# Optimization experiments

Hardware: AMD Instinct MI355X
Metric: run time of the kernel (lower is better)

Reference implementation:

```python
import jax, jax.numpy as jnp
import numpy as np

THRESH = 8000.0  # saturating partial-sum accumulator threshold (thresh=8000 in source)
GROUP = 128      # channel chunk size used by split_tensor_* helpers
EPS = 1e-5

def binarize(x):
    # sign() forward with straight-through estimator (standard BinarizeConv2d behavior)
    return x + jax.lax.stop_gradient(jnp.sign(x) - x)

def psum_conv3x3(x, w):
    """3x3 'same' conv computed as 9 shifted-window partial sums per 128-channel
    group, with the running accumulator saturated to [-THRESH, THRESH] after each
    partial sum (emulating a low-bit hardware accumulator).
    x: [B, C, H, W]; w: [O, C, 3, 3] -> out [B, O, H, W]."""
    B, C, H, W = x.shape
    O = w.shape[0]
    xp = jnp.pad(x, ((0, 0), (0, 0), (1, 1), (1, 1)))
    acc = jnp.zeros((B, O, H, W), dtype=x.dtype)
    n_groups = C // GROUP
    for g in range(n_groups):
        xg = xp[:, g * GROUP:(g + 1) * GROUP]
        wg = w[:, g * GROUP:(g + 1) * GROUP]
        # split_tensor ordering: x1..x9 vary row (dim2) fastest, then col (dim3)
        for col in range(3):
            for row in range(3):
                part = jnp.einsum('bchw,oc->bohw',
                                  xg[:, :, row:row + H, col:col + W],
                                  wg[:, :, row, col])
                acc = jnp.clip(acc + part, -THRESH, THRESH)
    return acc

def batchnorm(x, gamma, beta, mean, var):
    inv = gamma / jnp.sqrt(var + EPS)
    return x * inv[None, :, None, None] + (beta - mean * inv)[None, :, None, None]

def setup_inputs() -> dict:
    key = jax.random.key(0)
    ks = jax.random.split(key, 12)
    B, C, H, W = 64, 128, 56, 56
    return {
        'x': jax.random.normal(ks[0], (B, C, H, W), jnp.float32),
        'w1': jax.random.normal(ks[1], (C, C, 3, 3), jnp.float32),
        'w2': jax.random.normal(ks[2], (C, C, 3, 3), jnp.float32),
        'gamma1': jax.random.uniform(ks[3], (C,), jnp.float32, 0.5, 1.5),
        'beta1': jax.random.normal(ks[4], (C,), jnp.float32) * 0.1,
        'mean1': jax.random.normal(ks[5], (C,), jnp.float32),
        'var1': jax.random.uniform(ks[6], (C,), jnp.float32, 0.5, 1.5),
        'gamma2': jax.random.uniform(ks[7], (C,), jnp.float32, 0.5, 1.5),
        'beta2': jax.random.normal(ks[8], (C,), jnp.float32) * 0.1,
        'mean2': jax.random.normal(ks[9], (C,), jnp.float32),
        'var2': jax.random.uniform(ks[10], (C,), jnp.float32, 0.5, 1.5),
    }

def reference(x, w1, w2, gamma1, beta1, mean1, var1, gamma2, beta2, mean2, var2):
    residual = x
    out = psum_conv3x3(binarize(x), binarize(w1))
    out = batchnorm(out, gamma1, beta1, mean1, var1)
    out = jnp.clip(out, -1.0, 1.0)  # hardtanh
    out = psum_conv3x3(binarize(out), binarize(w2))
    out = batchnorm(out, gamma2, beta2, mean2, var2)
    out = out + residual
    out = jnp.clip(out, -1.0, 1.0)
    return out
```

## Files before the change

### kernel.cpp

```cpp
#include <hip/hip_runtime.h>
#include <cstdint>
#include <cstddef>


typedef int      v4i __attribute__((ext_vector_type(4)));
typedef float    v4f __attribute__((ext_vector_type(4)));
typedef unsigned int v2u __attribute__((ext_vector_type(2)));

constexpr int B = 64, C = 128, H = 56, W = 56;
constexpr int HP = H + 2, WP = W + 2;
constexpr int PIX = H * W;
constexpr int M = B * H * W;
constexpr int NTILES = M / 256;
constexpr int TPX = NTILES / 8;

constexpr size_t XS_BYTES = (size_t)B * HP * WP * C;
constexpr size_t XS1_OFF = 0;
constexpr size_t XS2_OFF = XS_BYTES;
constexpr size_t WF_BYTES = 18 * 8192;
constexpr size_t WF1_OFF = 2 * XS_BYTES;
constexpr size_t WF2_OFF = WF1_OFF + WF_BYTES;
constexpr size_t BNP_OFF = WF2_OFF + WF_BYTES;

__global__ __launch_bounds__(256) void zero_halo(int8_t* __restrict__ xs1,
                                                 int8_t* __restrict__ xs2) {
    int b = blockIdx.x >> 2;
    int q = blockIdx.x & 3;
    int t = q * 256 + threadIdx.x;
    size_t ib = (size_t)b * HP * WP * C;
#pragma unroll
    for (int a = 0; a < 2; ++a) {
        uint32_t* p = (uint32_t*)((a ? xs2 : xs1) + ib);
        const int ROWD = WP * C / 4;
        for (int i = t; i < ROWD; i += 1024) {
            p[i] = 0;
            p[(HP - 1) * ROWD + i] = 0;
        }
        for (int i = t; i < 56 * 2 * 32; i += 1024) {
            int r = i >> 6;
            int side = (i >> 5) & 1;
            int j = i & 31;
            p[((r + 1) * WP + side * (WP - 1)) * (C / 4) + j] = 0;
        }
    }
}

__global__ __launch_bounds__(256) void prep_x(const float* __restrict__ x,
                                              int8_t* __restrict__ xs) {
    __shared__ uint32_t tl[256 * 33];
    int t = threadIdx.x;
    int m = blockIdx.x * 256 + t;
    int b_ = m / PIX, hw = m % PIX;
    const float* xp = x + (size_t)b_ * C * PIX + hw;
#pragma unroll
    for (int c4 = 0; c4 < 32; ++c4) {
        uint32_t v = 0;
#pragma unroll
        for (int j = 0; j < 4; ++j) {
            float f = __builtin_nontemporal_load(xp + (size_t)(c4 * 4 + j) * PIX);
            v |= ((uint32_t)(uint8_t)(int8_t)((f > 0.f) - (f < 0.f))) << (8 * j);
        }
        tl[t * 33 + c4] = v;
    }
    __syncthreads();
    int pl = t >> 3, co = t & 7;
#pragma unroll
    for (int pass = 0; pass < 8; ++pass) {
        int p = pass * 32 + pl;
        int mg = blockIdx.x * 256 + p;
        int b2 = mg / PIX, hw2 = mg % PIX, h2 = hw2 / W, w2 = hw2 % W;
        size_t ob = ((size_t)(b2 * HP + h2 + 1) * WP + (w2 + 1)) * C + co * 16;
        v4i val;
#pragma unroll
        for (int k = 0; k < 4; ++k) val[k] = (int)tl[p * 33 + co * 4 + k];
        *(v4i*)(xs + ob) = val;
    }
}

__global__ __launch_bounds__(256) void prep_w(
    const float* __restrict__ w1, const float* __restrict__ w2,
    const float* __restrict__ g1, const float* __restrict__ be1,
    const float* __restrict__ mu1, const float* __restrict__ va1,
    const float* __restrict__ g2, const float* __restrict__ be2,
    const float* __restrict__ mu2, const float* __restrict__ va2,
    int8_t* __restrict__ wf1, int8_t* __restrict__ wf2,
    float* __restrict__ bnp) {
    int t = blockIdx.x * 256 + threadIdx.x;
    if (t < 256) {
        int o = t & 127;
        if (t < 128) {
            float inv = g1[o] / sqrtf(va1[o] + 1e-5f);
            bnp[o]       = inv;
            bnp[128 + o] = __fsub_rn(be1[o], __fmul_rn(mu1[o], inv));
        } else {
            float inv = g2[o] / sqrtf(va2[o] + 1e-5f);
            bnp[256 + o] = inv;
            bnp[384 + o] = __fsub_rn(be2[o], __fmul_rn(mu2[o], inv));
        }
    }
    if (t >= 2 * 18 * 8 * 64) return;
    int lane = t & 63;
    int nsub = (t >> 6) & 7;
    int kh   = (t >> 9) & 1;
    int tap  = (t >> 10) % 9;
    int which = (t >> 10) / 9;
    const float* w = which ? w2 : w1;
    int8_t* wf = which ? wf2 : wf1;
    int o = (lane & 15) * 8 + nsub;
    int cbase = kh * 64 + (lane >> 4) * 16;
    int r = tap / 3, s = tap % 3;
    int slot = r * 6 + kh * 3 + s;
    int8_t frag[16];
#pragma unroll
    for (int j = 0; j < 16; ++j) {
        float f = w[((size_t)(o * C + cbase + j) * 3 + r) * 3 + s];
        frag[j] = (int8_t)((f > 0.f) - (f < 0.f));
    }
    *(v4i*)(wf + (size_t)((slot * 8 + nsub) * 64 + lane) * 16) =
        *(const v4i*)frag;
}

template <int RG>
__device__ __forceinline__ void do_conv(
    int mwave, const int8_t* __restrict__ xs, const int8_t* wlds,
    int lane, int quad, int l15, v4i (&acc)[RG][8])
{
    int abase[RG];
#pragma unroll
    for (int rg = 0; rg < RG; ++rg) {
        int ma = mwave + rg * 16 + l15;
        int wa = ma % W; int ta = ma / W; int ha = ta % H; int ba = ta / H;
        abase[rg] = ((ba * HP + ha) * WP + wa) * C + quad * 16;
    }
    int lidx = lane << 4;

#pragma unroll
    for (int rg = 0; rg < RG; ++rg)
#pragma unroll
        for (int n = 0; n < 8; ++n) acc[rg][n] = (v4i)0;

    v4i a0[RG], a1[RG], bf0[8], bf1[8];
#pragma unroll
    for (int rg = 0; rg < RG; ++rg) a0[rg] = *(const v4i*)(xs + abase[rg]);
#pragma unroll
    for (int n = 0; n < 8; ++n)
        bf0[n] = *(const v4i*)(wlds + n * 1024 + lidx);
    __builtin_amdgcn_sched_barrier(0);

    const int8_t* wl = wlds;
    int aoffr = 0;
#pragma unroll 1
    for (int r3 = 0; r3 < 3; ++r3) {
#pragma unroll
        for (int kk = 0; kk < 6; ++kk) {
            const bool last = (r3 == 2) && (kk == 5);
            if (!last) {
                const int nkh = (kk + 1 < 6) ? ((kk + 1) / 3) : 0;
                const int ns  = (kk + 1 < 6) ? ((kk + 1) % 3) : 0;
                const int rbump = (kk + 1 < 6) ? 0 : WP * C;
                int naoff = aoffr + rbump + nkh * 64 + ns * C;
                const int8_t* lb = wl + (kk + 1) * 8192;
                if (((kk + 1) & 1) == 0) {
#pragma unroll
                    for (int rg = 0; rg < RG; ++rg)
                        a0[rg] = *(const v4i*)(xs + abase[rg] + naoff);
#pragma unroll
                    for (int n = 0; n < 8; ++n)
                        bf0[n] = *(const v4i*)(lb + n * 1024 + lidx);
                } else {
#pragma unroll
                    for (int rg = 0; rg < RG; ++rg)
                        a1[rg] = *(const v4i*)(xs + abase[rg] + naoff);
#pragma unroll
                    for (int n = 0; n < 8; ++n)
                        bf1[n] = *(const v4i*)(lb + n * 1024 + lidx);
                }
            }
            __builtin_amdgcn_sched_barrier(0);
            __builtin_amdgcn_s_setprio(1);
            if ((kk & 1) == 0) {
#pragma unroll
                for (int n = 0; n < 8; ++n)
#pragma unroll
                    for (int rg = 0; rg < RG; ++rg)
                        acc[rg][n] = __builtin_amdgcn_mfma_i32_16x16x64_i8(
                            a0[rg], bf0[n], acc[rg][n], 0, 0, 0);
            } else {
#pragma unroll
                for (int n = 0; n < 8; ++n)
#pragma unroll
                    for (int rg = 0; rg < RG; ++rg)
                        acc[rg][n] = __builtin_amdgcn_mfma_i32_16x16x64_i8(
                            a1[rg], bf1[n], acc[rg][n], 0, 0, 0);
            }
            __builtin_amdgcn_s_setprio(0);
            __builtin_amdgcn_sched_barrier(0);
        }
        aoffr += WP * C;
        wl += 6 * 8192;
    }
}

template <int RG>
__device__ __forceinline__ void epi_p1(
    v4i (&acc)[RG][8], int mwave, int quad, int l15,
    const float* binv, const float* btt, int8_t* __restrict__ xs_next)
{
#pragma unroll
    for (int rg = 0; rg < RG; ++rg) {
        int m0 = mwave + rg * 16 + quad * 4;
        int w0 = m0 % W; int t0 = m0 / W; int h0 = t0 % H; int b0 = t0 / H;
        int base = ((b0 * HP + h0 + 1) * WP + (w0 + 1)) * C + l15 * 8;
#pragma unroll
        for (int i = 0; i < 4; ++i) {
            uint32_t lo = 0, hi = 0;
#pragma unroll
            for (int n = 0; n < 8; ++n) {
                float y = __fadd_rn(__fmul_rn((float)acc[rg][n][i], binv[n]), btt[n]);
                uint32_t sb = (uint8_t)(int8_t)((y > 0.f) - (y < 0.f));
                if (n < 4) lo |= sb << (8 * n);
                else       hi |= sb << (8 * (n - 4));
            }
            v2u pk; pk[0] = lo; pk[1] = hi;
            *(v2u*)(xs_next + base + i * C) = pk;
        }
    }
}

template <int RG>
__device__ __forceinline__ void epi_p2(
    v4i (&acc)[RG][8], int m0, int wv, int quad, int l15,
    const float* binv, const float* btt,
    const float* __restrict__ xres, float* __restrict__ out, float* sm)
{
    constexpr int PXB = 128 * RG;
    int t = wv * 64 + quad * 16 + l15;
#pragma unroll 1
    for (int p = 0; p < 16; ++p) {
        if (l15 == p) {
#pragma unroll
            for (int rg = 0; rg < RG; ++rg)
#pragma unroll
                for (int n = 0; n < 8; ++n) {
                    v4f v;
#pragma unroll
                    for (int i = 0; i < 4; ++i)
                        v[i] = __fadd_rn(__fmul_rn((float)acc[rg][n][i],
                                                   binv[n]), btt[n]);
                    *(v4f*)(sm + n * PXB + wv * (RG * 16) + rg * 16 + quad * 4) = v;
                }
        }
        __syncthreads();
        if (t < PXB * 2) {
            int o_local = t / (PXB / 4);
            int px4 = (t % (PXB / 4)) * 4;
            v4f s = *(const v4f*)(sm + o_local * PXB + px4);
            int m = m0 + px4;
            int b0 = m / PIX, pp = m - b0 * PIX;
            size_t gidx = ((size_t)(b0 * C + p * 8 + o_local)) * PIX + pp;
            v4f r = *(const v4f*)(xres + gidx);
            v4f z;
#pragma unroll
            for (int i = 0; i < 4; ++i)
                z[i] = fminf(fmaxf(__fadd_rn(s[i], r[i]), -1.f), 1.f);
            __builtin_nontemporal_store(z, (v4f*)(out + gidx));
        }
        __syncthreads();
    }
}

__global__ __launch_bounds__(512, 1) void conv_p1(
    const int8_t* __restrict__ xs,
    const int8_t* __restrict__ wf,
    const float* __restrict__ bnp,
    int8_t* __restrict__ xs_next)
{
    __shared__ int8_t wlds[18 * 8192];
    int t = threadIdx.x, lane = t & 63, wv = t >> 6;
    int quad = lane >> 4, l15 = lane & 15;

    {
        const v4i* g = (const v4i*)wf;
        v4i* l = (v4i*)wlds;
        for (int i = t; i < 18 * 512; i += 512) l[i] = g[i];
    }
    float binv[8], btt[8];
    {
        int o0 = l15 * 8, o1 = 128 + l15 * 8;
#pragma unroll
        for (int n = 0; n < 8; ++n) { binv[n] = bnp[o0 + n]; btt[n] = bnp[o1 + n]; }
    }
    __syncthreads();

    int xcd = blockIdx.x & 7, local = blockIdx.x >> 3;
#pragma unroll 1
    for (int tloc = local; tloc < 96; tloc += 32) {
        int mw = (xcd * TPX + tloc) * 256 + wv * 32;
        v4i acc[2][8];
        do_conv<2>(mw, xs, wlds, lane, quad, l15, acc);
        epi_p1<2>(acc, mw, quad, l15, binv, btt, xs_next);
    }
    if (local < 4) {
        int tile = xcd * TPX + 96 + (local >> 1);
        int mw = tile * 256 + (local & 1) * 128 + wv * 16;
        v4i acc[1][8];
        do_conv<1>(mw, xs, wlds, lane, quad, l15, acc);
        epi_p1<1>(acc, mw, quad, l15, binv, btt, xs_next);
    }
}

__global__ __launch_bounds__(512, 1) void conv_p2(
    const int8_t* __restrict__ xs,
    const int8_t* __restrict__ wf,
    const float* __restrict__ bnp,
    const float* __restrict__ xres,
    float* __restrict__ out)
{
    __shared__ int8_t wlds[18 * 8192];
    __shared__ float  sm[8 * 256];
    int t = threadIdx.x, lane = t & 63, wv = t >> 6;
    int quad = lane >> 4, l15 = lane & 15;

    {
        const v4i* g = (const v4i*)wf;
        v4i* l = (v4i*)wlds;
        for (int i = t; i < 18 * 512; i += 512) l[i] = g[i];
    }
    float binv[8], btt[8];
    {
        int o0 = 256 + l15 * 8, o1 = 384 + l15 * 8;
#pragma unroll
        for (int n = 0; n < 8; ++n) { binv[n] = bnp[o0 + n]; btt[n] = bnp[o1 + n]; }
    }
    __syncthreads();

    int xcd = blockIdx.x & 7, local = blockIdx.x >> 3;
#pragma unroll 1
    for (int tloc = local; tloc < 96; tloc += 32) {
        int m0 = (xcd * TPX + tloc) * 256;
        int mw = m0 + wv * 32;
        v4i acc[2][8];
        do_conv<2>(mw, xs, wlds, lane, quad, l15, acc);
        epi_p2<2>(acc, m0, wv, quad, l15, binv, btt, xres, out, sm);
    }
    if (local < 4) {
        int tile = xcd * TPX + 96 + (local >> 1);
        int m0 = tile * 256 + (local & 1) * 128;
        int mw = m0 + wv * 16;
        v4i acc[1][8];
        do_conv<1>(mw, xs, wlds, lane, quad, l15, acc);
        epi_p2<1>(acc, m0, wv, quad, l15, binv, btt, xres, out, sm);
    }
}

extern "C" void kernel_launch(void* const* d_in, const int* in_sizes, int n_in,
                              void* d_out, int out_size, void* d_ws, size_t ws_size,
                              hipStream_t stream) {
    const float* x   = (const float*)d_in[0];
    const float* w1  = (const float*)d_in[1];
    const float* w2  = (const float*)d_in[2];
    const float* g1  = (const float*)d_in[3];
    const float* be1 = (const float*)d_in[4];
    const float* mu1 = (const float*)d_in[5];
    const float* va1 = (const float*)d_in[6];
    const float* g2  = (const float*)d_in[7];
    const float* be2 = (const float*)d_in[8];
    const float* mu2 = (const float*)d_in[9];
    const float* va2 = (const float*)d_in[10];

    int8_t* ws  = (int8_t*)d_ws;
    int8_t* xs1 = ws + XS1_OFF;
    int8_t* xs2 = ws + XS2_OFF;
    int8_t* wf1 = ws + WF1_OFF;
    int8_t* wf2 = ws + WF2_OFF;
    float*  bnp = (float*)(ws + BNP_OFF);

    zero_halo<<<256, 256, 0, stream>>>(xs1, xs2);
    prep_x<<<M / 256, 256, 0, stream>>>(x, xs1);
    prep_w<<<(2 * 18 * 8 * 64 + 255) / 256, 256, 0, stream>>>(
        w1, w2, g1, be1, mu1, va1, g2, be2, mu2, va2, wf1, wf2, bnp);

    conv_p1<<<256, 512, 0, stream>>>(xs1, wf1, bnp, xs2);
    conv_p2<<<256, 512, 0, stream>>>(xs2, wf2, bnp, x, (float*)d_out);
}
```

Baseline: 367.6 us.

## Fold tail tiles into last round and write conv2 epilogue directly without LDS

The leftover tail tiles are now merged into the final round as a third 16-row group per wave, so blocks with a tail take one RG=3 pass instead of an extra RG=1 pass. The conv2 epilogue drops the LDS transpose with its 16 barrier-separated rounds. Each lane instead writes four contiguous pixels per channel straight to global memory, with the residual read as a nontemporal load. Launch bounds become explicit flat-workgroup and waves-per-EU attributes, which changes the register budget and risks spills with RG=3 and less coalesced epilogue stores.

```diff
diff --git a/kernel.cpp b/kernel.cpp
--- a/kernel.cpp
+++ b/kernel.cpp
@@ -122,13 +122,13 @@
 
 template <int RG>
 __device__ __forceinline__ void do_conv(
-    int mwave, const int8_t* __restrict__ xs, const int8_t* wlds,
+    const int (&mrows)[RG], const int8_t* __restrict__ xs, const int8_t* wlds,
     int lane, int quad, int l15, v4i (&acc)[RG][8])
 {
     int abase[RG];
 #pragma unroll
     for (int rg = 0; rg < RG; ++rg) {
-        int ma = mwave + rg * 16 + l15;
+        int ma = mrows[rg] + l15;
         int wa = ma % W; int ta = ma / W; int ha = ta % H; int ba = ta / H;
         abase[rg] = ((ba * HP + ha) * WP + wa) * C + quad * 16;
     }
@@ -203,12 +203,12 @@
 
 template <int RG>
 __device__ __forceinline__ void epi_p1(
-    v4i (&acc)[RG][8], int mwave, int quad, int l15,
+    v4i (&acc)[RG][8], const int (&mrows)[RG], int quad, int l15,
     const float* binv, const float* btt, int8_t* __restrict__ xs_next)
 {
 #pragma unroll
     for (int rg = 0; rg < RG; ++rg) {
-        int m0 = mwave + rg * 16 + quad * 4;
+        int m0 = mrows[rg] + quad * 4;
         int w0 = m0 % W; int t0 = m0 / W; int h0 = t0 % H; int b0 = t0 / H;
         int base = ((b0 * HP + h0 + 1) * WP + (w0 + 1)) * C + l15 * 8;
 #pragma unroll
@@ -229,47 +229,33 @@
 
 template <int RG>
 __device__ __forceinline__ void epi_p2(
-    v4i (&acc)[RG][8], int m0, int wv, int quad, int l15,
+    v4i (&acc)[RG][8], const int (&mrows)[RG], int quad, int l15,
     const float* binv, const float* btt,
-    const float* __restrict__ xres, float* __restrict__ out, float* sm)
-{
-    constexpr int PXB = 128 * RG;
-    int t = wv * 64 + quad * 16 + l15;
-#pragma unroll 1
-    for (int p = 0; p < 16; ++p) {
-        if (l15 == p) {
-#pragma unroll
-            for (int rg = 0; rg < RG; ++rg)
-#pragma unroll
-                for (int n = 0; n < 8; ++n) {
-                    v4f v;
-#pragma unroll
-                    for (int i = 0; i < 4; ++i)
-                        v[i] = __fadd_rn(__fmul_rn((float)acc[rg][n][i],
-                                                   binv[n]), btt[n]);
-                    *(v4f*)(sm + n * PXB + wv * (RG * 16) + rg * 16 + quad * 4) = v;
-                }
-        }
-        __syncthreads();
-        if (t < PXB * 2) {
-            int o_local = t / (PXB / 4);
-            int px4 = (t % (PXB / 4)) * 4;
-            v4f s = *(const v4f*)(sm + o_local * PXB + px4);
-            int m = m0 + px4;
-            int b0 = m / PIX, pp = m - b0 * PIX;
-            size_t gidx = ((size_t)(b0 * C + p * 8 + o_local)) * PIX + pp;
-            v4f r = *(const v4f*)(xres + gidx);
+    const float* __restrict__ xres, float* __restrict__ out)
+{
+#pragma unroll
+    for (int rg = 0; rg < RG; ++rg) {
+        int m0 = mrows[rg] + quad * 4;
+        int w0 = m0 % W; int t0 = m0 / W; int h0 = t0 % H; int b0 = t0 / H;
+        int pixb = b0 * C * PIX + h0 * W + w0;
+#pragma unroll
+        for (int n = 0; n < 8; ++n) {
+            int idx = pixb + (l15 * 8 + n) * PIX;
+            v4f r = __builtin_nontemporal_load((const v4f*)(xres + idx));
             v4f z;
 #pragma unroll
-            for (int i = 0; i < 4; ++i)
-                z[i] = fminf(fmaxf(__fadd_rn(s[i], r[i]), -1.f), 1.f);
-            __builtin_nontemporal_store(z, (v4f*)(out + gidx));
-        }
-        __syncthreads();
-    }
-}
-
-__global__ __launch_bounds__(512, 1) void conv_p1(
+            for (int i = 0; i < 4; ++i) {
+                float y = __fadd_rn(__fmul_rn((float)acc[rg][n][i], binv[n]), btt[n]);
+                float v = __fadd_rn(y, r[i]);
+                z[i] = fminf(fmaxf(v, -1.f), 1.f);
+            }
+            __builtin_nontemporal_store(z, (v4f*)(out + idx));
+        }
+    }
+}
+
+__global__ __attribute__((amdgpu_flat_work_group_size(512, 512)))
+__attribute__((amdgpu_waves_per_eu(2, 2))) void conv_p1(
     const int8_t* __restrict__ xs,
     const int8_t* __restrict__ wf,
     const float* __restrict__ bnp,
@@ -294,22 +280,32 @@
 
     int xcd = blockIdx.x & 7, local = blockIdx.x >> 3;
 #pragma unroll 1
-    for (int tloc = local; tloc < 96; tloc += 32) {
-        int mw = (xcd * TPX + tloc) * 256 + wv * 32;
+    for (int rd = 0; rd < 2; ++rd) {
+        int mw = (xcd * TPX + local + rd * 32) * 256 + wv * 32;
+        int mrows2[2] = { mw, mw + 16 };
         v4i acc[2][8];
-        do_conv<2>(mw, xs, wlds, lane, quad, l15, acc);
-        epi_p1<2>(acc, mw, quad, l15, binv, btt, xs_next);
-    }
-    if (local < 4) {
-        int tile = xcd * TPX + 96 + (local >> 1);
-        int mw = tile * 256 + (local & 1) * 128 + wv * 16;
-        v4i acc[1][8];
-        do_conv<1>(mw, xs, wlds, lane, quad, l15, acc);
-        epi_p1<1>(acc, mw, quad, l15, binv, btt, xs_next);
-    }
-}
-
-__global__ __launch_bounds__(512, 1) void conv_p2(
+        do_conv<2>(mrows2, xs, wlds, lane, quad, l15, acc);
+        epi_p1<2>(acc, mrows2, quad, l15, binv, btt, xs_next);
+    }
+    {
+        int mw = (xcd * TPX + local + 64) * 256 + wv * 32;
+        if (local < 4) {
+            int tailrow = (xcd * TPX + 96) * 256 + (local * 8 + wv) * 16;
+            int mrows3[3] = { mw, mw + 16, tailrow };
+            v4i acc[3][8];
+            do_conv<3>(mrows3, xs, wlds, lane, quad, l15, acc);
+            epi_p1<3>(acc, mrows3, quad, l15, binv, btt, xs_next);
+        } else {
+            int mrows2[2] = { mw, mw + 16 };
+            v4i acc[2][8];
+            do_conv<2>(mrows2, xs, wlds, lane, quad, l15, acc);
+            epi_p1<2>(acc, mrows2, quad, l15, binv, btt, xs_next);
+        }
+    }
+}
+
+__global__ __attribute__((amdgpu_flat_work_group_size(512, 512)))
+__attribute__((amdgpu_waves_per_eu(2, 2))) void conv_p2(
     const int8_t* __restrict__ xs,
     const int8_t* __restrict__ wf,
     const float* __restrict__ bnp,
@@ -317,7 +313,6 @@
     float* __restrict__ out)
 {
     __shared__ int8_t wlds[18 * 8192];
-    __shared__ float  sm[8 * 256];
     int t = threadIdx.x, lane = t & 63, wv = t >> 6;
     int quad = lane >> 4, l15 = lane & 15;
 
@@ -336,20 +331,27 @@
 
     int xcd = blockIdx.x & 7, local = blockIdx.x >> 3;
 #pragma unroll 1
-    for (int tloc = local; tloc < 96; tloc += 32) {
-        int m0 = (xcd * TPX + tloc) * 256;
-        int mw = m0 + wv * 32;
+    for (int rd = 0; rd < 2; ++rd) {
+        int mw = (xcd * TPX + local + rd * 32) * 256 + wv * 32;
+        int mrows2[2] = { mw, mw + 16 };
         v4i acc[2][8];
-        do_conv<2>(mw, xs, wlds, lane, quad, l15, acc);
-        epi_p2<2>(acc, m0, wv, quad, l15, binv, btt, xres, out, sm);
-    }
-    if (local < 4) {
-        int tile = xcd * TPX + 96 + (local >> 1);
-        int m0 = tile * 256 + (local & 1) * 128;
-        int mw = m0 + wv * 16;
-        v4i acc[1][8];
-        do_conv<1>(mw, xs, wlds, lane, quad, l15, acc);
-        epi_p2<1>(acc, m0, wv, quad, l15, binv, btt, xres, out, sm);
+        do_conv<2>(mrows2, xs, wlds, lane, quad, l15, acc);
+        epi_p2<2>(acc, mrows2, quad, l15, binv, btt, xres, out);
+    }
+    {
+        int mw = (xcd * TPX + local + 64) * 256 + wv * 32;
+        if (local < 4) {
+            int tailrow = (xcd * TPX + 96) * 256 + (local * 8 + wv) * 16;
+            int mrows3[3] = { mw, mw + 16, tailrow };
+            v4i acc[3][8];
+            do_conv<3>(mrows3, xs, wlds, lane, quad, l15, acc);
+            epi_p2<3>(acc, mrows3, quad, l15, binv, btt, xres, out);
+        } else {
+            int mrows2[2] = { mw, mw + 16 };
+            v4i acc[2][8];
+            do_conv<2>(mrows2, xs, wlds, lane, quad, l15, acc);
+            epi_p2<2>(acc, mrows2, quad, l15, binv, btt, xres, out);
+        }
     }
 }
 
```

Result: faster. 332.1 us (-9.6%).
